# Performance work log

Hardware: AMD Instinct MI355X
Metric: run time of the kernel (lower is better)

Reference implementation:

```python
import jax, jax.numpy as jnp
import numpy as np

B, T, D, R = 4, 2048, 512, 1024
N_INNER, N_B = 9, 2          # inner pool bins, boundary pool bins (roipool_size='2_9')
RATIO = 1.0 / 5.0            # boundary extension ratio passed to BRoI1DPool
NB = N_B + N_INNER + N_B     # 13 total bins: [start bins | inner bins | end bins]


def _bin_centers(a, b, n):
    # a, b: (B, R) -> (B, R, n) centers of n equal bins covering [a, b]
    i = (jnp.arange(n, dtype=a.dtype) + 0.5) / n
    return a[..., None] + i * (b - a)[..., None]


def broi1d_pool(feats, rois):
    # Boundary ROI 1D pooling: feats (B, T, D), rois (B, R, 2) -> (B, R, D, NB).
    # Each bin samples its center position via linear interpolation along T.
    s, e = rois[..., 0], rois[..., 1]
    ext = RATIO * (e - s)
    pos = jnp.concatenate([
        _bin_centers(s - ext, s + ext, N_B),
        _bin_centers(s, e, N_INNER),
        _bin_centers(e - ext, e + ext, N_B)], axis=-1)          # (B, R, NB)
    pos = jnp.clip(pos, 0.0, T - 1)
    lo = jnp.floor(pos).astype(jnp.int32)
    hi = jnp.minimum(lo + 1, T - 1)
    w = (pos - lo.astype(pos.dtype))[..., None]

    def gather(idx):
        g = jnp.take_along_axis(feats, idx.reshape(idx.shape[0], -1)[..., None], axis=1)
        return g.reshape(idx.shape + (feats.shape[-1],))          # (B, R, NB, D)

    vals = (1.0 - w) * gather(lo) + w * gather(hi)
    return vals.transpose(0, 1, 3, 2)                              # (B, R, D, NB)


def setup_inputs():
    key = jax.random.key(0)
    ks = jax.random.split(key, 10)
    features = jax.random.normal(ks[0], (B, T, D), jnp.float32)

    def make_rois(k):
        k1, k2 = jax.random.split(k)
        s = jax.random.uniform(k1, (B, R), jnp.float32, 0.0, T - 300.0)
        L = 16.0 + jax.random.uniform(k2, (B, R), jnp.float32) * 256.0
        return jnp.stack([s, s + L], axis=-1)

    rois = make_rois(ks[1])
    start_rois = make_rois(ks[2])
    end_rois = make_rois(ks[3])
    rois_mask = jnp.ones((B, R), jnp.float32)
    rois_pos_emb = jax.random.normal(ks[4], (B, R, D), jnp.float32)

    d_left = (N_B + N_INNER // 2 + 1) * D
    W_left = jax.random.normal(ks[5], (D, d_left), jnp.float32) / np.sqrt(d_left).astype(np.float32)
    b_left = jnp.zeros((D,), jnp.float32)
    W_inner = jax.random.normal(ks[6], (D, N_INNER * D), jnp.float32) / np.sqrt(N_INNER * D).astype(np.float32)
    b_inner = jnp.zeros((D,), jnp.float32)
    W_roi = jax.random.normal(ks[7], (D, 2 * D), jnp.float32) / np.sqrt(2 * D).astype(np.float32)
    b_roi = jnp.zeros((D,), jnp.float32)
    return {"features": features, "start_rois": start_rois, "end_rois": end_rois,
            "rois": rois, "rois_mask": rois_mask, "rois_pos_emb": rois_pos_emb,
            "W_left": W_left, "b_left": b_left, "W_inner": W_inner, "b_inner": b_inner,
            "W_roi": W_roi, "b_roi": b_roi}


def reference(features, start_rois, end_rois, rois, rois_mask, rois_pos_emb,
              W_left, b_left, W_inner, b_inner, W_roi, b_roi):
    pooled = broi1d_pool(features, rois)          # (B, R, D, NB)
    mb, r = pooled.shape[:2]

    def fc(x, W, b):
        # Linear + Dropout(eval=identity) + SELU
        return jax.nn.selu(x @ W.T + b)

    left = fc(pooled[:, :, :, 0:N_INNER // 2 + N_B + 1].reshape(mb, r, -1), W_left, b_left)
    inner = fc(pooled[:, :, :, N_B:N_INNER + N_B].reshape(mb, r, -1), W_inner, b_inner)
    # NOTE: the original code reuses left_fc for the right branch (right_fc is dead).
    right = fc(pooled[:, :, :, N_INNER // 2 + N_B:N_INNER + 2 * N_B].reshape(mb, r, -1), W_left, b_left)
    return fc(jnp.concatenate([right - left, inner], axis=2), W_roi, b_roi)  # (B, R, D)
```

## Files before the change

### kernel.cpp

```cpp
#include <hip/hip_runtime.h>
#include <hip/hip_bf16.h>
#include <cstdint>
#include <cmath>

#define BB 4
#define TT 2048
#define DD 512
#define RR 1024
#define MM (BB*RR)
#define NBINS 13
#define LDXP (NBINS*DD)

typedef __bf16 bf16;
typedef bf16 bf16x8 __attribute__((ext_vector_type(8)));
typedef float f32x4 __attribute__((ext_vector_type(4)));

__device__ __forceinline__ float selu_f(float x) {
    const float sc = 1.0507009873554805f;
    const float aa = 1.6732632423543772f;
    return x > 0.0f ? sc * x : sc * aa * (expf(x) - 1.0f);
}

__device__ __forceinline__ void gload_lds16(const bf16* g, bf16* l) {
    __builtin_amdgcn_global_load_lds(
        (const __attribute__((address_space(1))) void*)g,
        (__attribute__((address_space(3))) void*)l, 16, 0, 0);
}

template<int N>
__device__ __forceinline__ void wait_vm() {
    if constexpr (N == 0)      asm volatile("s_waitcnt vmcnt(0)" ::: "memory");
    else if constexpr (N == 6) asm volatile("s_waitcnt vmcnt(6)" ::: "memory");
    else if constexpr (N == 8) asm volatile("s_waitcnt vmcnt(8)" ::: "memory");
}

template<int ROWS>
__device__ __forceinline__ void stage_tile64(const bf16* __restrict__ src, int lda,
                                             bf16* tile, int tid) {
#pragma unroll
    for (int it = 0; it < ROWS / 32; ++it) {
        int idx = it * 256 + tid;
        int row = idx >> 3;
        int col = ((idx & 7) ^ (row & 7)) * 8;
        bf16* wavebase = tile + (idx & ~63) * 8;
        gload_lds16(src + (size_t)row * lda + col, wavebase);
    }
}

__device__ __forceinline__ bf16x8 frd64(const bf16* tile, int row, int s) {
    int p = s ^ (row & 7);
    return *(const bf16x8*)(tile + row * 64 + p * 8);
}

template<int NB_, int KT>
__device__ __forceinline__ void w_row_body(const float* __restrict__ Wsrc,
                                           bf16* __restrict__ Wdst,
                                           float* ld, int n, int tid) {
    const float* src = Wsrc + (size_t)n * KT;
    for (int i = tid; i < KT; i += 256) ld[i] = src[i];
    __syncthreads();
    bf16* dst = Wdst + (size_t)n * KT;
    for (int i = tid; i < KT; i += 256) {
        int bin = i >> 9, d = i & 511;
        dst[i] = (bf16)ld[d * NB_ + bin];
    }
}

__device__ __forceinline__ void pool_body(const float* __restrict__ feats,
                                          const float* __restrict__ rois,
                                          bf16* __restrict__ Xp, int m, int tid) {
    int b = m >> 10;
    float s = rois[2 * m];
    float e = rois[2 * m + 1];
    float ext = 0.2f * (e - s);
    int dd = (tid & 63) * 8;
    int j0 = tid >> 6;
    const float* fb = feats + (size_t)b * TT * DD + dd;
    bf16* orow = Xp + (size_t)m * LDXP + dd;
#pragma unroll
    for (int jj = 0; jj < 4; ++jj) {
        int j = j0 + jj * 4;
        if (j >= NBINS) break;
        float pos;
        if (j < 2)       pos = (s - ext) + ((float)j + 0.5f) * ext;
        else if (j < 11) pos = s + (((float)(j - 2) + 0.5f) * (1.0f / 9.0f)) * (e - s);
        else             pos = (e - ext) + ((float)(j - 11) + 0.5f) * ext;
        pos = fminf(fmaxf(pos, 0.0f), (float)(TT - 1));
        float fl = floorf(pos);
        int lo = (int)fl;
        int hi = lo + 1; if (hi > TT - 1) hi = TT - 1;
        float w = pos - fl;
        const float* rlo = fb + (size_t)lo * DD;
        const float* rhi = fb + (size_t)hi * DD;
        float4 l0 = *(const float4*)(rlo);
        float4 l1 = *(const float4*)(rlo + 4);
        float4 h0 = *(const float4*)(rhi);
        float4 h1 = *(const float4*)(rhi + 4);
        bf16x8 o;
        o[0] = (bf16)((1.0f - w) * l0.x + w * h0.x);
        o[1] = (bf16)((1.0f - w) * l0.y + w * h0.y);
        o[2] = (bf16)((1.0f - w) * l0.z + w * h0.z);
        o[3] = (bf16)((1.0f - w) * l0.w + w * h0.w);
        o[4] = (bf16)((1.0f - w) * l1.x + w * h1.x);
        o[5] = (bf16)((1.0f - w) * l1.y + w * h1.y);
        o[6] = (bf16)((1.0f - w) * l1.z + w * h1.z);
        o[7] = (bf16)((1.0f - w) * l1.w + w * h1.w);
        *(bf16x8*)(orow + j * DD) = o;
    }
}

__global__ __launch_bounds__(256) void prep_all(
    const float* __restrict__ feats, const float* __restrict__ rois,
    const float* __restrict__ W_left, const float* __restrict__ W_inner,
    const float* __restrict__ W_roi,
    bf16* __restrict__ Xp, bf16* __restrict__ Wl, bf16* __restrict__ Wi,
    bf16* __restrict__ Wr)
{
    __shared__ float ld[4608];
    int bid = blockIdx.x, tid = threadIdx.x;
    if (bid < 4096) {
        pool_body(feats, rois, Xp, bid, tid);
    } else if (bid < 4608) {
        w_row_body<7, 3584>(W_left, Wl, ld, bid - 4096, tid);
    } else if (bid < 5120) {
        w_row_body<9, 4608>(W_inner, Wi, ld, bid - 4608, tid);
    } else {
        int i0 = (bid - 5120) * 1024 + tid * 4;
        float4 v = *(const float4*)(W_roi + i0);
        bf16* d = Wr + i0;
        d[0] = (bf16)v.x; d[1] = (bf16)v.y; d[2] = (bf16)v.z; d[3] = (bf16)v.w;
    }
}


template<int K, bool OUT_BF16>
__device__ __forceinline__ void gemm_single_body(
    const bf16* __restrict__ A, int lda,
    const bf16* __restrict__ Bw, const float* __restrict__ bias,
    void* __restrict__ Out, int ldo, int ocol0,
    bf16* sm, int m0, int n0)
{
    int tid = threadIdx.x, lane = tid & 63, w = tid >> 6;
    int wr = w >> 1, wc = w & 1;
    const bf16* Ab = A + (size_t)m0 * lda;
    const bf16* Bb = Bw + (size_t)n0 * K;
    int frow = lane & 15, sl = lane >> 4;
    f32x4 acc[2][4] = {};
    bf16 *A0 = sm,         *B0 = sm + 4096;
    bf16 *A1 = sm + 12288, *B1 = sm + 12288 + 4096;

    auto stage = [&](bf16* as, bf16* bs, int t) {
        stage_tile64<64>(Ab + t * 64, lda, as, tid);
        stage_tile64<128>(Bb + t * 64, K, bs, tid);
    };
    auto step_body = [&](bf16* as, bf16* bs, int t, bool dostage) {
        __builtin_amdgcn_s_barrier();
        bf16x8 af[2][2], bfr[2][4];
#pragma unroll
        for (int ks = 0; ks < 2; ++ks) {
#pragma unroll
            for (int mf = 0; mf < 2; ++mf) af[ks][mf] = frd64(as, wr * 32 + mf * 16 + frow, ks * 4 + sl);
#pragma unroll
            for (int nf = 0; nf < 4; ++nf) bfr[ks][nf] = frd64(bs, wc * 64 + nf * 16 + frow, ks * 4 + sl);
        }
        asm volatile("s_waitcnt lgkmcnt(0)" ::: "memory");
        __builtin_amdgcn_sched_barrier(0);
        __builtin_amdgcn_s_barrier();
        if (dostage) stage(as, bs, t + 2);
        __builtin_amdgcn_s_setprio(1);
#pragma unroll
        for (int ks = 0; ks < 2; ++ks)
#pragma unroll
            for (int mf = 0; mf < 2; ++mf)
#pragma unroll
                for (int nf = 0; nf < 4; ++nf)
                    acc[mf][nf] = __builtin_amdgcn_mfma_f32_16x16x32_bf16(af[ks][mf], bfr[ks][nf], acc[mf][nf], 0, 0, 0);
        __builtin_amdgcn_s_setprio(0);
    };

    constexpr int NT = K / 64;
    stage(A0, B0, 0);
    stage(A1, B1, 1);
    for (int t = 0; t + 2 < NT; t += 2) {
        wait_vm<6>(); step_body(A0, B0, t, true);
        wait_vm<6>(); step_body(A1, B1, t + 1, true);
    }
    wait_vm<6>(); step_body(A0, B0, NT - 2, false);
    wait_vm<0>(); step_body(A1, B1, NT - 1, false);

    int crow = (lane >> 4) * 4;
    int ccol = lane & 15;
#pragma unroll
    for (int mf = 0; mf < 2; ++mf) {
#pragma unroll
        for (int nf = 0; nf < 4; ++nf) {
            int col = n0 + wc * 64 + nf * 16 + ccol;
            float bv = bias[col];
#pragma unroll
            for (int r2 = 0; r2 < 4; ++r2) {
                int row = m0 + wr * 32 + mf * 16 + crow + r2;
                float v = selu_f(acc[mf][nf][r2] + bv);
                if constexpr (OUT_BF16)
                    ((bf16*)Out)[(size_t)row * ldo + ocol0 + col] = (bf16)v;
                else
                    ((float*)Out)[(size_t)row * ldo + ocol0 + col] = v;
            }
        }
    }
}

template<int K>
__device__ __forceinline__ void gemm_dual_body(
    const bf16* __restrict__ Xp, const bf16* __restrict__ Wl,
    const float* __restrict__ bias, bf16* __restrict__ Y,
    bf16* sm, int m0, int n0)
{
    int tid = threadIdx.x, lane = tid & 63, w = tid >> 6;
    int wr = w >> 1, wc = w & 1;
    const bf16* AL = Xp + (size_t)m0 * LDXP;
    const bf16* AR = AL + 3072;
    const bf16* Bb = Wl + (size_t)n0 * K;
    int frow = lane & 15, sl = lane >> 4;
    f32x4 accL[2][4] = {}, accR[2][4] = {};
    bf16 *L0 = sm,         *R0 = sm + 4096,         *B0 = sm + 8192;
    bf16 *L1 = sm + 16384, *R1 = sm + 16384 + 4096, *B1 = sm + 16384 + 8192;

    auto stage = [&](bf16* ls, bf16* rs, bf16* bs, int t) {
        stage_tile64<64>(AL + t * 64, LDXP, ls, tid);
        stage_tile64<64>(AR + t * 64, LDXP, rs, tid);
        stage_tile64<128>(Bb + t * 64, K, bs, tid);
    };
    auto step_body = [&](bf16* ls, bf16* rs, bf16* bs, int t, bool dostage) {
        __builtin_amdgcn_s_barrier();
        bf16x8 afL[2][2], afR[2][2], bfr[2][4];
#pragma unroll
        for (int ks = 0; ks < 2; ++ks) {
#pragma unroll
            for (int mf = 0; mf < 2; ++mf) {
                afL[ks][mf] = frd64(ls, wr * 32 + mf * 16 + frow, ks * 4 + sl);
                afR[ks][mf] = frd64(rs, wr * 32 + mf * 16 + frow, ks * 4 + sl);
            }
#pragma unroll
            for (int nf = 0; nf < 4; ++nf) bfr[ks][nf] = frd64(bs, wc * 64 + nf * 16 + frow, ks * 4 + sl);
        }
        asm volatile("s_waitcnt lgkmcnt(0)" ::: "memory");
        __builtin_amdgcn_sched_barrier(0);
        __builtin_amdgcn_s_barrier();
        if (dostage) stage(ls, rs, bs, t + 2);
        __builtin_amdgcn_s_setprio(1);
#pragma unroll
        for (int ks = 0; ks < 2; ++ks)
#pragma unroll
            for (int mf = 0; mf < 2; ++mf)
#pragma unroll
                for (int nf = 0; nf < 4; ++nf) {
                    accL[mf][nf] = __builtin_amdgcn_mfma_f32_16x16x32_bf16(afL[ks][mf], bfr[ks][nf], accL[mf][nf], 0, 0, 0);
                    accR[mf][nf] = __builtin_amdgcn_mfma_f32_16x16x32_bf16(afR[ks][mf], bfr[ks][nf], accR[mf][nf], 0, 0, 0);
                }
        __builtin_amdgcn_s_setprio(0);
    };

    constexpr int NT = K / 64;
    stage(L0, R0, B0, 0);
    stage(L1, R1, B1, 1);
    for (int t = 0; t + 2 < NT; t += 2) {
        wait_vm<8>(); step_body(L0, R0, B0, t, true);
        wait_vm<8>(); step_body(L1, R1, B1, t + 1, true);
    }
    wait_vm<8>(); step_body(L0, R0, B0, NT - 2, false);
    wait_vm<0>(); step_body(L1, R1, B1, NT - 1, false);

    int crow = (lane >> 4) * 4;
    int ccol = lane & 15;
#pragma unroll
    for (int mf = 0; mf < 2; ++mf) {
#pragma unroll
        for (int nf = 0; nf < 4; ++nf) {
            int col = n0 + wc * 64 + nf * 16 + ccol;
            float bv = bias[col];
#pragma unroll
            for (int r2 = 0; r2 < 4; ++r2) {
                int row = m0 + wr * 32 + mf * 16 + crow + r2;
                float vL = selu_f(accL[mf][nf][r2] + bv);
                float vR = selu_f(accR[mf][nf][r2] + bv);
                Y[(size_t)row * 1024 + col] = (bf16)(vR - vL);
            }
        }
    }
}

__global__ __launch_bounds__(256) void wide_gemm(
    const bf16* __restrict__ Xp, const bf16* __restrict__ Wl,
    const float* __restrict__ bl, const bf16* __restrict__ Wi,
    const float* __restrict__ bi, bf16* __restrict__ Y)
{
    __shared__ bf16 sm[32768];
    int bid = blockIdx.x;
    if (bid < 256) {
        gemm_dual_body<3584>(Xp, Wl, bl, Y, sm, (bid & 63) * 64, (bid >> 6) * 128);
    } else {
        int b2 = bid - 256;
        gemm_single_body<4608, true>(Xp + 1024, LDXP, Wi, bi, (void*)Y, 1024, 512,
                                     sm, (b2 & 63) * 64, (b2 >> 6) * 128);
    }
}

__global__ __launch_bounds__(256) void final_gemm(
    const bf16* __restrict__ Y, const bf16* __restrict__ Wr,
    const float* __restrict__ br, float* __restrict__ out)
{
    __shared__ bf16 sm[24576];
    int bid = blockIdx.x;
    gemm_single_body<1024, false>(Y, 1024, Wr, br, (void*)out, 512, 0,
                                  sm, (bid & 63) * 64, (bid >> 6) * 128);
}

extern "C" void kernel_launch(void* const* d_in, const int* in_sizes, int n_in,
                              void* d_out, int out_size, void* d_ws, size_t ws_size,
                              hipStream_t stream) {
    const float* feats   = (const float*)d_in[0];
    const float* rois    = (const float*)d_in[3];
    const float* W_left  = (const float*)d_in[6];
    const float* b_left  = (const float*)d_in[7];
    const float* W_inner = (const float*)d_in[8];
    const float* b_inner = (const float*)d_in[9];
    const float* W_roi   = (const float*)d_in[10];
    const float* b_roi   = (const float*)d_in[11];
    float* out = (float*)d_out;

    bf16* wsb = (bf16*)d_ws;
    constexpr size_t XP_ELEMS = (size_t)MM * LDXP;
    constexpr size_t WL_ELEMS = (size_t)512 * 3584;
    constexpr size_t WI_ELEMS = (size_t)512 * 4608;
    constexpr size_t WR_ELEMS = (size_t)512 * 1024;
    bf16* Xp = wsb;
    bf16* Wl = Xp + XP_ELEMS;
    bf16* Wi = Wl + WL_ELEMS;
    bf16* Wr = Wi + WI_ELEMS;
    bf16* Y  = Wr + WR_ELEMS;

    prep_all<<<5632, 256, 0, stream>>>(feats, rois, W_left, W_inner, W_roi,
                                       Xp, Wl, Wi, Wr);
    wide_gemm<<<512, 256, 0, stream>>>(Xp, Wl, b_left, Wi, b_inner, Y);
    final_gemm<<<256, 256, 0, stream>>>(Y, Wr, b_roi, out);
}
```

Measured before the change: 101.7 us.

## Restructure GEMM mainloops into 4-stage K=32 pipeline with register double-buffered fragments

Replaces the 2-stage K=64 LDS double buffer in both GEMM bodies with a 4-slot ring of K=32 tiles staged three steps ahead, using a new swizzle for 32-wide rows. Each iteration prefetches the next step's fragments from LDS into a second register set while issuing MFMAs on the current set. This needs only one barrier per step, so LDS reads overlap with matrix math and there is deeper global-load lookahead. In exchange it adds more barriers per unit of K, holds more fragment registers live, and changes the LDS footprint.

```diff
diff --git a/kernel.cpp b/kernel.cpp
--- a/kernel.cpp
+++ b/kernel.cpp
@@ -30,26 +30,37 @@
 template<int N>
 __device__ __forceinline__ void wait_vm() {
     if constexpr (N == 0)      asm volatile("s_waitcnt vmcnt(0)" ::: "memory");
+    else if constexpr (N == 3) asm volatile("s_waitcnt vmcnt(3)" ::: "memory");
+    else if constexpr (N == 4) asm volatile("s_waitcnt vmcnt(4)" ::: "memory");
     else if constexpr (N == 6) asm volatile("s_waitcnt vmcnt(6)" ::: "memory");
     else if constexpr (N == 8) asm volatile("s_waitcnt vmcnt(8)" ::: "memory");
 }
 
+__device__ __forceinline__ void lgkm_fence() {
+    asm volatile("s_waitcnt lgkmcnt(0)" ::: "memory");
+    __builtin_amdgcn_sched_barrier(0);
+}
+__device__ __forceinline__ void barrier_pinned() {
+    __builtin_amdgcn_s_barrier();
+    __builtin_amdgcn_sched_barrier(0);
+}
+
 template<int ROWS>
-__device__ __forceinline__ void stage_tile64(const bf16* __restrict__ src, int lda,
-                                             bf16* tile, int tid) {
-#pragma unroll
-    for (int it = 0; it < ROWS / 32; ++it) {
+__device__ __forceinline__ void stage32(const bf16* __restrict__ src, int lda,
+                                        bf16* dst, int tid) {
+#pragma unroll
+    for (int it = 0; it < (ROWS * 4) / 256; ++it) {
         int idx = it * 256 + tid;
-        int row = idx >> 3;
-        int col = ((idx & 7) ^ (row & 7)) * 8;
-        bf16* wavebase = tile + (idx & ~63) * 8;
+        int row = idx >> 2;
+        int col = ((idx & 3) ^ ((row >> 1) & 3)) * 8;
+        bf16* wavebase = dst + (idx & ~63) * 8;
         gload_lds16(src + (size_t)row * lda + col, wavebase);
     }
 }
 
-__device__ __forceinline__ bf16x8 frd64(const bf16* tile, int row, int s) {
-    int p = s ^ (row & 7);
-    return *(const bf16x8*)(tile + row * 64 + p * 8);
+__device__ __forceinline__ bf16x8 frd32(const bf16* tile, int row, int sl) {
+    int p = sl ^ ((row >> 1) & 3);
+    return *(const bf16x8*)(tile + row * 32 + p * 8);
 }
 
 template<int NB_, int KT>
@@ -146,47 +157,49 @@
     const bf16* Bb = Bw + (size_t)n0 * K;
     int frow = lane & 15, sl = lane >> 4;
     f32x4 acc[2][4] = {};
-    bf16 *A0 = sm,         *B0 = sm + 4096;
-    bf16 *A1 = sm + 12288, *B1 = sm + 12288 + 4096;
-
-    auto stage = [&](bf16* as, bf16* bs, int t) {
-        stage_tile64<64>(Ab + t * 64, lda, as, tid);
-        stage_tile64<128>(Bb + t * 64, K, bs, tid);
-    };
-    auto step_body = [&](bf16* as, bf16* bs, int t, bool dostage) {
-        __builtin_amdgcn_s_barrier();
-        bf16x8 af[2][2], bfr[2][4];
-#pragma unroll
-        for (int ks = 0; ks < 2; ++ks) {
-#pragma unroll
-            for (int mf = 0; mf < 2; ++mf) af[ks][mf] = frd64(as, wr * 32 + mf * 16 + frow, ks * 4 + sl);
-#pragma unroll
-            for (int nf = 0; nf < 4; ++nf) bfr[ks][nf] = frd64(bs, wc * 64 + nf * 16 + frow, ks * 4 + sl);
-        }
-        asm volatile("s_waitcnt lgkmcnt(0)" ::: "memory");
-        __builtin_amdgcn_sched_barrier(0);
-        __builtin_amdgcn_s_barrier();
-        if (dostage) stage(as, bs, t + 2);
+
+    auto stage = [&](int u) {
+        bf16* p = sm + (u & 3) * 6144;
+        stage32<64>(Ab + u * 32, lda, p, tid);
+        stage32<128>(Bb + u * 32, K, p + 2048, tid);
+    };
+    bf16x8 fA[2][2], fB[2][4];
+    auto readf = [&](int u, int s) {
+        bf16* p = sm + (u & 3) * 6144;
+#pragma unroll
+        for (int mf = 0; mf < 2; ++mf) fA[s][mf] = frd32(p, wr * 32 + mf * 16 + frow, sl);
+#pragma unroll
+        for (int nf = 0; nf < 4; ++nf) fB[s][nf] = frd32(p + 2048, wc * 64 + nf * 16 + frow, sl);
+    };
+    auto mma = [&](int s) {
         __builtin_amdgcn_s_setprio(1);
 #pragma unroll
-        for (int ks = 0; ks < 2; ++ks)
-#pragma unroll
-            for (int mf = 0; mf < 2; ++mf)
-#pragma unroll
-                for (int nf = 0; nf < 4; ++nf)
-                    acc[mf][nf] = __builtin_amdgcn_mfma_f32_16x16x32_bf16(af[ks][mf], bfr[ks][nf], acc[mf][nf], 0, 0, 0);
+        for (int mf = 0; mf < 2; ++mf)
+#pragma unroll
+            for (int nf = 0; nf < 4; ++nf)
+                acc[mf][nf] = __builtin_amdgcn_mfma_f32_16x16x32_bf16(fA[s][mf], fB[s][nf], acc[mf][nf], 0, 0, 0);
         __builtin_amdgcn_s_setprio(0);
     };
 
-    constexpr int NT = K / 64;
-    stage(A0, B0, 0);
-    stage(A1, B1, 1);
-    for (int t = 0; t + 2 < NT; t += 2) {
-        wait_vm<6>(); step_body(A0, B0, t, true);
-        wait_vm<6>(); step_body(A1, B1, t + 1, true);
-    }
-    wait_vm<6>(); step_body(A0, B0, NT - 2, false);
-    wait_vm<0>(); step_body(A1, B1, NT - 1, false);
+    constexpr int NT = K / 32;
+    auto body = [&](int t, int cs, int fs) {
+        if (t + 2 < NT) wait_vm<3>(); else wait_vm<0>();
+        barrier_pinned();
+        if (t + 3 < NT) stage(t + 3);
+        if (t + 1 < NT) readf(t + 1, fs);
+        mma(cs);
+        lgkm_fence();
+    };
+
+    stage(0); stage(1); stage(2);
+    wait_vm<6>();
+    barrier_pinned();
+    readf(0, 0);
+    lgkm_fence();
+    for (int t = 0; t < NT; t += 2) {
+        body(t, 0, 1);
+        body(t + 1, 1, 0);
+    }
 
     int crow = (lane >> 4) * 4;
     int ccol = lane & 15;
@@ -222,53 +235,56 @@
     const bf16* Bb = Wl + (size_t)n0 * K;
     int frow = lane & 15, sl = lane >> 4;
     f32x4 accL[2][4] = {}, accR[2][4] = {};
-    bf16 *L0 = sm,         *R0 = sm + 4096,         *B0 = sm + 8192;
-    bf16 *L1 = sm + 16384, *R1 = sm + 16384 + 4096, *B1 = sm + 16384 + 8192;
-
-    auto stage = [&](bf16* ls, bf16* rs, bf16* bs, int t) {
-        stage_tile64<64>(AL + t * 64, LDXP, ls, tid);
-        stage_tile64<64>(AR + t * 64, LDXP, rs, tid);
-        stage_tile64<128>(Bb + t * 64, K, bs, tid);
-    };
-    auto step_body = [&](bf16* ls, bf16* rs, bf16* bs, int t, bool dostage) {
-        __builtin_amdgcn_s_barrier();
-        bf16x8 afL[2][2], afR[2][2], bfr[2][4];
-#pragma unroll
-        for (int ks = 0; ks < 2; ++ks) {
-#pragma unroll
-            for (int mf = 0; mf < 2; ++mf) {
-                afL[ks][mf] = frd64(ls, wr * 32 + mf * 16 + frow, ks * 4 + sl);
-                afR[ks][mf] = frd64(rs, wr * 32 + mf * 16 + frow, ks * 4 + sl);
+
+    auto stage = [&](int u) {
+        bf16* p = sm + (u & 3) * 8192;
+        stage32<64>(AL + u * 32, LDXP, p, tid);
+        stage32<64>(AR + u * 32, LDXP, p + 2048, tid);
+        stage32<128>(Bb + u * 32, K, p + 4096, tid);
+    };
+    bf16x8 fL[2][2], fR[2][2], fB[2][4];
+    auto readf = [&](int u, int s) {
+        bf16* p = sm + (u & 3) * 8192;
+#pragma unroll
+        for (int mf = 0; mf < 2; ++mf) {
+            fL[s][mf] = frd32(p, wr * 32 + mf * 16 + frow, sl);
+            fR[s][mf] = frd32(p + 2048, wr * 32 + mf * 16 + frow, sl);
+        }
+#pragma unroll
+        for (int nf = 0; nf < 4; ++nf)
+            fB[s][nf] = frd32(p + 4096, wc * 64 + nf * 16 + frow, sl);
+    };
+    auto mma = [&](int s) {
+        __builtin_amdgcn_s_setprio(1);
+#pragma unroll
+        for (int mf = 0; mf < 2; ++mf)
+#pragma unroll
+            for (int nf = 0; nf < 4; ++nf) {
+                accL[mf][nf] = __builtin_amdgcn_mfma_f32_16x16x32_bf16(fL[s][mf], fB[s][nf], accL[mf][nf], 0, 0, 0);
+                accR[mf][nf] = __builtin_amdgcn_mfma_f32_16x16x32_bf16(fR[s][mf], fB[s][nf], accR[mf][nf], 0, 0, 0);
             }
-#pragma unroll
-            for (int nf = 0; nf < 4; ++nf) bfr[ks][nf] = frd64(bs, wc * 64 + nf * 16 + frow, ks * 4 + sl);
-        }
-        asm volatile("s_waitcnt lgkmcnt(0)" ::: "memory");
-        __builtin_amdgcn_sched_barrier(0);
-        __builtin_amdgcn_s_barrier();
-        if (dostage) stage(ls, rs, bs, t + 2);
-        __builtin_amdgcn_s_setprio(1);
-#pragma unroll
-        for (int ks = 0; ks < 2; ++ks)
-#pragma unroll
-            for (int mf = 0; mf < 2; ++mf)
-#pragma unroll
-                for (int nf = 0; nf < 4; ++nf) {
-                    accL[mf][nf] = __builtin_amdgcn_mfma_f32_16x16x32_bf16(afL[ks][mf], bfr[ks][nf], accL[mf][nf], 0, 0, 0);
-                    accR[mf][nf] = __builtin_amdgcn_mfma_f32_16x16x32_bf16(afR[ks][mf], bfr[ks][nf], accR[mf][nf], 0, 0, 0);
-                }
         __builtin_amdgcn_s_setprio(0);
     };
 
-    constexpr int NT = K / 64;
-    stage(L0, R0, B0, 0);
-    stage(L1, R1, B1, 1);
-    for (int t = 0; t + 2 < NT; t += 2) {
-        wait_vm<8>(); step_body(L0, R0, B0, t, true);
-        wait_vm<8>(); step_body(L1, R1, B1, t + 1, true);
-    }
-    wait_vm<8>(); step_body(L0, R0, B0, NT - 2, false);
-    wait_vm<0>(); step_body(L1, R1, B1, NT - 1, false);
+    constexpr int NT = K / 32;
+    auto body = [&](int t, int cs, int fs) {
+        if (t + 2 < NT) wait_vm<4>(); else wait_vm<0>();
+        barrier_pinned();
+        if (t + 3 < NT) stage(t + 3);
+        if (t + 1 < NT) readf(t + 1, fs);
+        mma(cs);
+        lgkm_fence();
+    };
+
+    stage(0); stage(1); stage(2);
+    wait_vm<8>();
+    barrier_pinned();
+    readf(0, 0);
+    lgkm_fence();
+    for (int t = 0; t < NT; t += 2) {
+        body(t, 0, 1);
+        body(t + 1, 1, 0);
+    }
 
     int crow = (lane >> 4) * 4;
     int ccol = lane & 15;
```

Result: slower. 118.0 us (+16.0%).

## Software-pipeline LDS fragment reads with MFMA in dual-branch GEMM

Applied to the files above, without the earlier changes.

Splits each K-step of the left/right dual GEMM into interleaved phases. LDS reads for the next half (L+B, then R) are issued while the MFMAs for the previous half run, using double-buffered register fragments. Staging is also split so the L tile is refilled separately from the R and B tiles, with more barriers placed between phases. The wide GEMM kernel now requests two blocks per CU via launch bounds. This caps registers and risks spilling, given the larger fragment arrays and the 64 accumulator registers.

```diff
diff --git a/kernel.cpp b/kernel.cpp
--- a/kernel.cpp
+++ b/kernel.cpp
@@ -132,7 +132,6 @@
     }
 }
 
-
 template<int K, bool OUT_BF16>
 __device__ __forceinline__ void gemm_single_body(
     const bf16* __restrict__ A, int lda,
@@ -222,53 +221,91 @@
     const bf16* Bb = Wl + (size_t)n0 * K;
     int frow = lane & 15, sl = lane >> 4;
     f32x4 accL[2][4] = {}, accR[2][4] = {};
-    bf16 *L0 = sm,         *R0 = sm + 4096,         *B0 = sm + 8192;
-    bf16 *L1 = sm + 16384, *R1 = sm + 16384 + 4096, *B1 = sm + 16384 + 8192;
-
-    auto stage = [&](bf16* ls, bf16* rs, bf16* bs, int t) {
-        stage_tile64<64>(AL + t * 64, LDXP, ls, tid);
-        stage_tile64<64>(AR + t * 64, LDXP, rs, tid);
-        stage_tile64<128>(Bb + t * 64, K, bs, tid);
-    };
-    auto step_body = [&](bf16* ls, bf16* rs, bf16* bs, int t, bool dostage) {
-        __builtin_amdgcn_s_barrier();
-        bf16x8 afL[2][2], afR[2][2], bfr[2][4];
+    bf16 *Ls[2] = {sm,         sm + 4096};
+    bf16 *Rs[2] = {sm + 8192,  sm + 12288};
+    bf16 *Bs[2] = {sm + 16384, sm + 24576};
+
+    bf16x8 fL[2][2][2], fR[2][2][2], fB[2][2][4];
+
+    auto stageL  = [&](int t) {
+        stage_tile64<64>(AL + t * 64, LDXP, Ls[t & 1], tid);
+    };
+    auto stageRB = [&](int t) {
+        stage_tile64<64>(AR + t * 64, LDXP, Rs[t & 1], tid);
+        stage_tile64<128>(Bb + t * 64, K, Bs[t & 1], tid);
+    };
+    auto readLB = [&](int t, int s) {
 #pragma unroll
         for (int ks = 0; ks < 2; ++ks) {
 #pragma unroll
-            for (int mf = 0; mf < 2; ++mf) {
-                afL[ks][mf] = frd64(ls, wr * 32 + mf * 16 + frow, ks * 4 + sl);
-                afR[ks][mf] = frd64(rs, wr * 32 + mf * 16 + frow, ks * 4 + sl);
-            }
-#pragma unroll
-            for (int nf = 0; nf < 4; ++nf) bfr[ks][nf] = frd64(bs, wc * 64 + nf * 16 + frow, ks * 4 + sl);
+            for (int nf = 0; nf < 4; ++nf)
+                fB[s][ks][nf] = frd64(Bs[t & 1], wc * 64 + nf * 16 + frow, ks * 4 + sl);
+#pragma unroll
+            for (int mf = 0; mf < 2; ++mf)
+                fL[s][ks][mf] = frd64(Ls[t & 1], wr * 32 + mf * 16 + frow, ks * 4 + sl);
         }
-        asm volatile("s_waitcnt lgkmcnt(0)" ::: "memory");
-        __builtin_amdgcn_sched_barrier(0);
-        __builtin_amdgcn_s_barrier();
-        if (dostage) stage(ls, rs, bs, t + 2);
+    };
+    auto readR = [&](int t, int s) {
+#pragma unroll
+        for (int ks = 0; ks < 2; ++ks)
+#pragma unroll
+            for (int mf = 0; mf < 2; ++mf)
+                fR[s][ks][mf] = frd64(Rs[t & 1], wr * 32 + mf * 16 + frow, ks * 4 + sl);
+    };
+    auto mmaR = [&](int s) {
         __builtin_amdgcn_s_setprio(1);
 #pragma unroll
         for (int ks = 0; ks < 2; ++ks)
 #pragma unroll
             for (int mf = 0; mf < 2; ++mf)
 #pragma unroll
-                for (int nf = 0; nf < 4; ++nf) {
-                    accL[mf][nf] = __builtin_amdgcn_mfma_f32_16x16x32_bf16(afL[ks][mf], bfr[ks][nf], accL[mf][nf], 0, 0, 0);
-                    accR[mf][nf] = __builtin_amdgcn_mfma_f32_16x16x32_bf16(afR[ks][mf], bfr[ks][nf], accR[mf][nf], 0, 0, 0);
-                }
+                for (int nf = 0; nf < 4; ++nf)
+                    accR[mf][nf] = __builtin_amdgcn_mfma_f32_16x16x32_bf16(fR[s][ks][mf], fB[s][ks][nf], accR[mf][nf], 0, 0, 0);
         __builtin_amdgcn_s_setprio(0);
     };
+    auto mmaL = [&](int s) {
+        __builtin_amdgcn_s_setprio(1);
+#pragma unroll
+        for (int ks = 0; ks < 2; ++ks)
+#pragma unroll
+            for (int mf = 0; mf < 2; ++mf)
+#pragma unroll
+                for (int nf = 0; nf < 4; ++nf)
+                    accL[mf][nf] = __builtin_amdgcn_mfma_f32_16x16x32_bf16(fL[s][ks][mf], fB[s][ks][nf], accL[mf][nf], 0, 0, 0);
+        __builtin_amdgcn_s_setprio(0);
+    };
 
     constexpr int NT = K / 64;
-    stage(L0, R0, B0, 0);
-    stage(L1, R1, B1, 1);
-    for (int t = 0; t + 2 < NT; t += 2) {
-        wait_vm<8>(); step_body(L0, R0, B0, t, true);
-        wait_vm<8>(); step_body(L1, R1, B1, t + 1, true);
-    }
-    wait_vm<8>(); step_body(L0, R0, B0, NT - 2, false);
-    wait_vm<0>(); step_body(L1, R1, B1, NT - 1, false);
+    stageL(0); stageRB(0); stageL(1); stageRB(1);
+
+    for (int t = 0; t < NT; t += 2) {
+        if (t + 1 < NT) wait_vm<8>(); else wait_vm<0>();
+        __builtin_amdgcn_s_barrier();
+        readLB(t, 0);
+        if (t > 0) mmaR(1);
+        asm volatile("s_waitcnt lgkmcnt(0)" ::: "memory");
+        __builtin_amdgcn_s_barrier();
+        if (t + 2 < NT) stageL(t + 2);
+        readR(t, 0);
+        mmaL(0);
+        asm volatile("s_waitcnt lgkmcnt(0)" ::: "memory");
+        __builtin_amdgcn_s_barrier();
+        if (t + 2 < NT) stageRB(t + 2);
+        int t1 = t + 1;
+        if (t1 + 1 < NT) wait_vm<8>(); else wait_vm<0>();
+        __builtin_amdgcn_s_barrier();
+        readLB(t1, 1);
+        mmaR(0);
+        asm volatile("s_waitcnt lgkmcnt(0)" ::: "memory");
+        __builtin_amdgcn_s_barrier();
+        if (t1 + 2 < NT) stageL(t1 + 2);
+        readR(t1, 1);
+        mmaL(1);
+        asm volatile("s_waitcnt lgkmcnt(0)" ::: "memory");
+        __builtin_amdgcn_s_barrier();
+        if (t1 + 2 < NT) stageRB(t1 + 2);
+    }
+    mmaR(1);
 
     int crow = (lane >> 4) * 4;
     int ccol = lane & 15;
@@ -289,7 +326,7 @@
     }
 }
 
-__global__ __launch_bounds__(256) void wide_gemm(
+__global__ __launch_bounds__(256, 2) void wide_gemm(
     const bf16* __restrict__ Xp, const bf16* __restrict__ Wl,
     const float* __restrict__ bl, const bf16* __restrict__ Wi,
     const float* __restrict__ bi, bf16* __restrict__ Y)
```

After: 99.74 us. Within noise of the previous version (-2.0%).
